# Kernel optimization log

Measured on AMD Instinct MI355X. Metric: run time of the kernel, lower is better.

The kernel has to match this reference:

```python
import jax, jax.numpy as jnp
import numpy as np


def _pairwise_sqdist(x, y):
    # x: [B, N, 3], y: [B, M, 3] -> squared L2 distances [B, N, M]
    x2 = jnp.sum(x * x, axis=-1)  # [B, N]
    y2 = jnp.sum(y * y, axis=-1)  # [B, M]
    xy = jnp.einsum('bnd,bmd->bnm', x, y)  # [B, N, M]
    d2 = x2[:, :, None] + y2[:, None, :] - 2.0 * xy
    return jnp.maximum(d2, 0.0)


def setup_inputs() -> dict:
    key = jax.random.key(0)
    kx, ky = jax.random.split(key)
    B, N, M, D = 4, 4096, 4096, 3
    x = jax.random.normal(kx, (B, N, D), dtype=jnp.float32)
    y = jax.random.normal(ky, (B, M, D), dtype=jnp.float32)
    return {"x": x, "y": y}


def reference(x, y):
    # Single-directional chamfer, pytorch3d defaults:
    # squared-L2 NN dist, mean over points, mean over batch -> scalar.
    d2 = _pairwise_sqdist(x, y)  # [B, N, M]
    # x -> y: for each x point, min over y points
    x_to_y = jnp.mean(jnp.min(d2, axis=2))
    # y -> x: for each y point, min over x points (reuse same matrix)
    y_to_x = jnp.mean(jnp.min(d2, axis=1))
    return jnp.maximum(x_to_y, y_to_x)
```

## Files before the change

kernel.cpp:

```cpp
#include <hip/hip_runtime.h>

#define B_   4
#define N_   4096
#define BN_  (B_ * N_)
#define TPB  256
#define PT   8
#define QS   128


__device__ __forceinline__ unsigned enc_ord(float f) {
    int b = __float_as_int(f);
    return (unsigned)(b ^ ((b >> 31) | 0x80000000));
}
__device__ __forceinline__ float dec_ord(unsigned u) {
    int b = (u & 0x80000000u) ? (int)(u ^ 0x80000000u) : ~(int)u;
    return __int_as_float(b);
}

__global__ __launch_bounds__(TPB) void pack_kernel(
    const float* __restrict__ x, const float* __restrict__ y,
    float4* __restrict__ pk, unsigned* __restrict__ mins)
{
    const int gid = blockIdx.x * TPB + threadIdx.x;
    const float* src = (gid < BN_) ? x : y;
    const int idx = gid & (BN_ - 1);
    const float a0 = src[idx * 3 + 0];
    const float a1 = src[idx * 3 + 1];
    const float a2 = src[idx * 3 + 2];
    const float hqq = 0.5f * (a0 * a0 + a1 * a1 + a2 * a2);
    pk[gid] = make_float4(a0, a1, a2, hqq);
    mins[gid] = 0xFFFFFFFFu;
}

__global__ __launch_bounds__(TPB) void chamfer_kernel(
    const float4* __restrict__ pk, unsigned* __restrict__ mins)
{
    __shared__ float4 sQ[QS];

    const int z    = blockIdx.z;
    const int b    = z & (B_ - 1);
    const bool swp = z >= B_;
    const float4* pkP = pk + (swp ? BN_ : 0) + b * N_;
    const float4* pkQ = pk + (swp ? 0 : BN_) + b * N_;
    unsigned*    omin = mins + (swp ? BN_ : 0) + b * N_;

    const int tid = threadIdx.x;
    if (tid < QS) sQ[tid] = pkQ[blockIdx.x * QS + tid];

    const int n0 = blockIdx.y * (PT * TPB) + tid;
    float4 p[PT];
    float  m[PT];
    #pragma unroll
    for (int k = 0; k < PT; ++k) {
        p[k] = pkP[n0 + k * TPB];
        m[k] = 3.4e38f;
    }
    __syncthreads();

    #pragma unroll 8
    for (int j = 0; j < QS; ++j) {
        const float4 qq = sQ[j];
        #pragma unroll
        for (int k = 0; k < PT; ++k) {
            const float e = fmaf(-p[k].x, qq.x,
                            fmaf(-p[k].y, qq.y,
                            fmaf(-p[k].z, qq.z, qq.w)));
            m[k] = fminf(m[k], e);
        }
    }

    #pragma unroll
    for (int k = 0; k < PT; ++k)
        atomicMin(&omin[n0 + k * TPB], enc_ord((m[k] + p[k].w) * 2.0f));
}

__global__ __launch_bounds__(1024) void finalize_kernel(
    const unsigned* __restrict__ mins, float* __restrict__ out)
{
    const int tid = threadIdx.x;
    const uint4* m4 = (const uint4*)mins;
    float s0 = 0.0f, s1 = 0.0f;
    #pragma unroll
    for (int i = 0; i < BN_ / 4; i += 1024) {
        const uint4 a = m4[i + tid];
        s0 += fmaxf(dec_ord(a.x), 0.0f) + fmaxf(dec_ord(a.y), 0.0f)
            + fmaxf(dec_ord(a.z), 0.0f) + fmaxf(dec_ord(a.w), 0.0f);
        const uint4 c = m4[BN_ / 4 + i + tid];
        s1 += fmaxf(dec_ord(c.x), 0.0f) + fmaxf(dec_ord(c.y), 0.0f)
            + fmaxf(dec_ord(c.z), 0.0f) + fmaxf(dec_ord(c.w), 0.0f);
    }
    #pragma unroll
    for (int o = 32; o > 0; o >>= 1) {
        s0 += __shfl_down(s0, o);
        s1 += __shfl_down(s1, o);
    }
    __shared__ float w0[16], w1[16];
    const int w = tid >> 6;
    if ((tid & 63) == 0) { w0[w] = s0; w1[w] = s1; }
    __syncthreads();
    if (tid == 0) {
        float t0 = 0.0f, t1 = 0.0f;
        #pragma unroll
        for (int i = 0; i < 16; ++i) { t0 += w0[i]; t1 += w1[i]; }
        const float inv = 1.0f / (float)BN_;
        out[0] = fmaxf(t0 * inv, t1 * inv);
    }
}

extern "C" void kernel_launch(void* const* d_in, const int* in_sizes, int n_in,
                              void* d_out, int out_size, void* d_ws, size_t ws_size,
                              hipStream_t stream)
{
    const float* x = (const float*)d_in[0];
    const float* y = (const float*)d_in[1];
    float* out = (float*)d_out;

    float4*   pk   = (float4*)d_ws;
    unsigned* mins = (unsigned*)(pk + 2 * BN_);

    pack_kernel<<<2 * BN_ / TPB, TPB, 0, stream>>>(x, y, pk, mins);

    dim3 grid(N_ / QS, N_ / (PT * TPB), 2 * B_);
    chamfer_kernel<<<grid, TPB, 0, stream>>>(pk, mins);

    finalize_kernel<<<1, 1024, 0, stream>>>(mins, out);
}
```

Before: 72.85 us.

## Fuse finalize reduction into chamfer kernel via last-block counter; halve Q tile

Removes the separate finalize launch: each chamfer block increments a global counter after its atomicMin writes, and the last block to finish reads all per-point minima and produces the scalar output. The counter is reset in the pack kernel. The Q tile size is also halved to 64, doubling the grid and the number of atomicMin passes. In exchange, the final reduction runs on a single 256-thread block with scalar atomic loads instead of 1024 threads with vector loads, and every block pays a fence and an extra atomic.

```diff
diff --git a/kernel.cpp b/kernel.cpp
--- a/kernel.cpp
+++ b/kernel.cpp
@@ -5,7 +5,8 @@
 #define BN_  (B_ * N_)
 #define TPB  256
 #define PT   8
-#define QS   128
+#define QS   64
+#define NBLK (2 * B_ * (N_ / QS) * (N_ / (PT * TPB)))
 
 
 __device__ __forceinline__ unsigned enc_ord(float f) {
@@ -19,9 +20,11 @@
 
 __global__ __launch_bounds__(TPB) void pack_kernel(
     const float* __restrict__ x, const float* __restrict__ y,
-    float4* __restrict__ pk, unsigned* __restrict__ mins)
+    float4* __restrict__ pk, unsigned* __restrict__ mins,
+    unsigned* __restrict__ counter)
 {
     const int gid = blockIdx.x * TPB + threadIdx.x;
+    if (gid == 0) *counter = 0u;
     const float* src = (gid < BN_) ? x : y;
     const int idx = gid & (BN_ - 1);
     const float a0 = src[idx * 3 + 0];
@@ -33,7 +36,8 @@
 }
 
 __global__ __launch_bounds__(TPB) void chamfer_kernel(
-    const float4* __restrict__ pk, unsigned* __restrict__ mins)
+    const float4* __restrict__ pk, unsigned* __restrict__ mins,
+    unsigned* __restrict__ counter, float* __restrict__ out)
 {
     __shared__ float4 sQ[QS];
 
@@ -72,36 +76,35 @@
     #pragma unroll
     for (int k = 0; k < PT; ++k)
         atomicMin(&omin[n0 + k * TPB], enc_ord((m[k] + p[k].w) * 2.0f));
-}
 
-__global__ __launch_bounds__(1024) void finalize_kernel(
-    const unsigned* __restrict__ mins, float* __restrict__ out)
-{
-    const int tid = threadIdx.x;
-    const uint4* m4 = (const uint4*)mins;
+    __threadfence();
+    __syncthreads();
+    __shared__ unsigned s_last;
+    if (tid == 0) s_last = atomicAdd(counter, 1u);
+    __syncthreads();
+    if (s_last != NBLK - 1) return;
+
     float s0 = 0.0f, s1 = 0.0f;
-    #pragma unroll
-    for (int i = 0; i < BN_ / 4; i += 1024) {
-        const uint4 a = m4[i + tid];
-        s0 += fmaxf(dec_ord(a.x), 0.0f) + fmaxf(dec_ord(a.y), 0.0f)
-            + fmaxf(dec_ord(a.z), 0.0f) + fmaxf(dec_ord(a.w), 0.0f);
-        const uint4 c = m4[BN_ / 4 + i + tid];
-        s1 += fmaxf(dec_ord(c.x), 0.0f) + fmaxf(dec_ord(c.y), 0.0f)
-            + fmaxf(dec_ord(c.z), 0.0f) + fmaxf(dec_ord(c.w), 0.0f);
+    for (int i = tid; i < BN_; i += TPB) {
+        const unsigned a = __hip_atomic_load(&mins[i], __ATOMIC_RELAXED,
+                                             __HIP_MEMORY_SCOPE_AGENT);
+        const unsigned c = __hip_atomic_load(&mins[BN_ + i], __ATOMIC_RELAXED,
+                                             __HIP_MEMORY_SCOPE_AGENT);
+        s0 += fmaxf(dec_ord(a), 0.0f);
+        s1 += fmaxf(dec_ord(c), 0.0f);
     }
     #pragma unroll
     for (int o = 32; o > 0; o >>= 1) {
         s0 += __shfl_down(s0, o);
         s1 += __shfl_down(s1, o);
     }
-    __shared__ float w0[16], w1[16];
+    __shared__ float w0[4], w1[4];
     const int w = tid >> 6;
     if ((tid & 63) == 0) { w0[w] = s0; w1[w] = s1; }
     __syncthreads();
     if (tid == 0) {
-        float t0 = 0.0f, t1 = 0.0f;
-        #pragma unroll
-        for (int i = 0; i < 16; ++i) { t0 += w0[i]; t1 += w1[i]; }
+        const float t0 = w0[0] + w0[1] + w0[2] + w0[3];
+        const float t1 = w1[0] + w1[1] + w1[2] + w1[3];
         const float inv = 1.0f / (float)BN_;
         out[0] = fmaxf(t0 * inv, t1 * inv);
     }
@@ -115,13 +118,12 @@
     const float* y = (const float*)d_in[1];
     float* out = (float*)d_out;
 
-    float4*   pk   = (float4*)d_ws;
-    unsigned* mins = (unsigned*)(pk + 2 * BN_);
+    float4*   pk      = (float4*)d_ws;
+    unsigned* mins    = (unsigned*)(pk + 2 * BN_);
+    unsigned* counter = mins + 2 * BN_;
 
-    pack_kernel<<<2 * BN_ / TPB, TPB, 0, stream>>>(x, y, pk, mins);
+    pack_kernel<<<2 * BN_ / TPB, TPB, 0, stream>>>(x, y, pk, mins, counter);
 
     dim3 grid(N_ / QS, N_ / (PT * TPB), 2 * B_);
-    chamfer_kernel<<<grid, TPB, 0, stream>>>(pk, mins);
-
-    finalize_kernel<<<1, 1024, 0, stream>>>(mins, out);
+    chamfer_kernel<<<grid, TPB, 0, stream>>>(pk, mins, counter, out);
 }
```

New measurement: 137.8 us. 89.1% more time.
